# Performance work log

Measured on AMD Instinct MI355X. Metric: run time of the kernel, lower is better.

The kernel has to match this reference:

```python
import jax, jax.numpy as jnp
import numpy as np

BANDLIMIT = 0.5
STEP_SCALE = 1.0  # refiner default step_scale_value
LN_EPS = 1e-5


def _layernorm(x, g, b):
    mu = jnp.mean(x, axis=-1, keepdims=True)
    xc = x - mu
    inv = jax.lax.rsqrt(jnp.mean(xc * xc, axis=-1, keepdims=True) + LN_EPS)
    return xc * inv * g + b


def setup_inputs() -> dict:
    key = jax.random.key(0)
    ks = jax.random.split(key, 12)
    B, C, H, W = 16, 384, 64, 64
    P = 192  # conj-sym half of state_dim=384
    x = jax.random.normal(ks[0], (B, C, H, W), dtype=jnp.float32)
    ln1_g = 1.0 + 0.1 * jax.random.normal(ks[1], (C,), dtype=jnp.float32)
    ln1_b = 0.1 * jax.random.normal(ks[2], (C,), dtype=jnp.float32)
    # stable diagonal A: negative real part, HiPPO-like imaginary ladder
    lam_re = -(0.3 + jax.random.uniform(ks[3], (P,), dtype=jnp.float32))
    lam_im = jnp.pi * jnp.arange(P, dtype=jnp.float32)
    Lambda = jnp.stack([lam_re, lam_im], axis=-1)          # [P,2] (re,im)
    Bmat = jax.random.normal(ks[4], (P, C, 2), dtype=jnp.float32) / np.sqrt(C)
    Cmat = jax.random.normal(ks[5], (C, P, 2), dtype=jnp.float32) / np.sqrt(P)
    D = jax.random.normal(ks[6], (C,), dtype=jnp.float32)
    log_step = jax.random.uniform(ks[7], (P,), dtype=jnp.float32,
                                  minval=float(np.log(1e-3)), maxval=float(np.log(0.1)))
    ln2_g = 1.0 + 0.1 * jax.random.normal(ks[8], (C,), dtype=jnp.float32)
    ln2_b = 0.1 * jax.random.normal(ks[9], (C,), dtype=jnp.float32)
    W_enc = jax.random.normal(ks[10], (2 * C, C), dtype=jnp.float32) / np.sqrt(C)
    W_dec = jax.random.normal(ks[11], (C, C), dtype=jnp.float32) / np.sqrt(C)
    return {"x": x, "ln1_g": ln1_g, "ln1_b": ln1_b, "Lambda": Lambda,
            "Bmat": Bmat, "Cmat": Cmat, "D": D, "log_step": log_step,
            "ln2_g": ln2_g, "ln2_b": ln2_b, "W_enc": W_enc, "W_dec": W_dec}


def reference(x, ln1_g, ln1_b, Lambda, Bmat, Cmat, D, log_step, ln2_g, ln2_b, W_enc, W_dec):
    Bsz, C, H, W = x.shape
    u = x.reshape(Bsz, C, H * W).transpose(0, 2, 1)        # [B, L, C]

    # --- S5Block: attn branch ---
    fx = _layernorm(u, ln1_g, ln1_b)
    res = fx

    lam = Lambda[..., 0] + 1j * Lambda[..., 1]             # [P] complex
    Bc = Bmat[..., 0] + 1j * Bmat[..., 1]                  # [P, C]
    Cc = Cmat[..., 0] + 1j * Cmat[..., 1]                  # [C, P]
    step = STEP_SCALE * jnp.exp(log_step)                  # [P]
    # bandlimit mask on C (as in S5 with bandlimit=0.5)
    freqs = (step / STEP_SCALE) * jnp.abs(Lambda[..., 1]) / (2.0 * jnp.pi)
    mask = (freqs < BANDLIMIT * 0.5).astype(Cc.dtype)
    Cc = Cc * mask
    # ZOH discretization
    lam_bar = jnp.exp(lam * step)                          # [P]
    B_bar = ((lam_bar - 1.0) / lam)[:, None] * Bc          # [P, C]
    Bu = jnp.einsum('ph,blh->blp', B_bar, fx.astype(B_bar.dtype))  # [B,L,P] complex
    lam_el = jnp.broadcast_to(lam_bar, Bu.shape)

    def binop(a, b):
        # linear recurrence composition: x <- a2*(a1*x + b1) + b2
        return a[0] * b[0], b[0] * a[1] + b[1]

    _, xs = jax.lax.associative_scan(binop, (lam_el, Bu), axis=1)  # [B,L,P]
    y = 2.0 * jnp.real(jnp.einsum('hp,blp->blh', Cc, xs)) + D * fx
    y = jax.nn.gelu(y, approximate=False) + res

    # --- S5Block: GEGLU FFN branch ---
    fy = _layernorm(y, ln2_g, ln2_b)
    z = fy @ W_enc.T                                       # [B,L,2C]
    z1, z2 = jnp.split(z, 2, axis=-1)
    z = z1 * jax.nn.gelu(z2, approximate=False)
    y = z @ W_dec.T + fy

    return y.transpose(0, 2, 1).reshape(Bsz, C, H, W)
```

## Files before the change

kernel.cpp:

```cpp
#include <hip/hip_runtime.h>
#include <hip/hip_bf16.h>
#include <math.h>

typedef __attribute__((ext_vector_type(4))) float f32x4;
typedef __attribute__((ext_vector_type(8))) short s16x8;
typedef unsigned short u16;
typedef unsigned int u32;

#define CDIM 384
#define PDIM 192
#define LDIM 4096
#define BSZ  16
#define MDIM 65536
#define KD   384
#define BM 128
#define BN 128
#define BK 32
#define NT (KD / BK)
#define BUFE (BM * BK)

__device__ __forceinline__ u16 f2bf(float f) {
    u32 x = __float_as_uint(f);
    x += 0x7fffu + ((x >> 16) & 1u);
    return (u16)(x >> 16);
}
__device__ __forceinline__ float bf2f(u16 v) {
    return __uint_as_float(((u32)v) << 16);
}
__device__ __forceinline__ float gelu_exact(float x) {
    return 0.5f * x * (1.0f + erff(x * 0.7071067811865476f));
}
__device__ __forceinline__ float gelu_fast(float x) {
    float w = -1.5957691216f * x * (1.0f + 0.044715f * x * x);
    return x / (1.0f + __expf(w));
}
__device__ __forceinline__ void gld_lds16(const u16* g, u16* l) {
    __builtin_amdgcn_global_load_lds(
        (const __attribute__((address_space(1))) void*)g,
        (__attribute__((address_space(3))) void*)l, 16, 0, 0);
}

__device__ __forceinline__ void swz_decode(int NY, int& mt, int& nt) {
    int bid = blockIdx.x + gridDim.x * blockIdx.y;
    int nwg = gridDim.x * gridDim.y;
    int cpx = nwg >> 3;
    int work = (bid & 7) * cpx + (bid >> 3);
    mt = work / NY;
    nt = work - mt * NY;
}

__global__ __launch_bounds__(256) void k_setup(
    const float* __restrict__ Lambda, const float* __restrict__ Bmat,
    const float* __restrict__ Cmat, const float* __restrict__ log_step,
    const float* __restrict__ W_enc, const float* __restrict__ W_dec,
    u16* __restrict__ Wb, u16* __restrict__ Wc, u16* __restrict__ We,
    u16* __restrict__ Wd, float* __restrict__ lam_bar)
{
    int idx = blockIdx.x * 256 + threadIdx.x;
    if (idx < 73728) {
        int p = idx / CDIM, c = idx % CDIM;
        float st  = expf(log_step[p]);
        float lre = Lambda[2*p], lim = Lambda[2*p+1];
        float el  = expf(lre * st);
        float lbr = el * cosf(lim * st);
        float lbi = el * sinf(lim * st);
        float dd  = lre*lre + lim*lim;
        float a = lbr - 1.0f, b = lbi;
        float cr = (a * lre + b * lim) / dd;
        float ci = (b * lre - a * lim) / dd;
        float Br = Bmat[2*(p*CDIM + c)], Bi = Bmat[2*(p*CDIM + c) + 1];
        Wb[p*KD + c]          = f2bf(cr*Br - ci*Bi);
        Wb[(PDIM + p)*KD + c] = f2bf(cr*Bi + ci*Br);
    } else if (idx < 147456) {
        int e = idx - 73728;
        int h = e / PDIM, p = e % PDIM;
        float st  = expf(log_step[p]);
        float lim = Lambda[2*p+1];
        float freq = st * fabsf(lim) / 6.283185307179586f;
        float sc = (freq < 0.25f) ? 2.0f : 0.0f;
        Wc[h*KD + p]        = f2bf( sc * Cmat[2*(h*PDIM + p)]);
        Wc[h*KD + PDIM + p] = f2bf(-sc * Cmat[2*(h*PDIM + p) + 1]);
    } else if (idx < 442368) {
        int e = idx - 147456;
        We[e] = f2bf(W_enc[e]);
    } else if (idx < 589824) {
        int e = idx - 442368;
        Wd[e] = f2bf(W_dec[e]);
    } else if (idx < 590016) {
        int p = idx - 589824;
        float st  = expf(log_step[p]);
        float lre = Lambda[2*p], lim = Lambda[2*p+1];
        float el  = expf(lre * st);
        lam_bar[2*p]   = el * cosf(lim * st);
        lam_bar[2*p+1] = el * sinf(lim * st);
    }
}

#define LNS 388
__global__ __launch_bounds__(256) void k_ln1(
    const float* __restrict__ x, const float* __restrict__ g,
    const float* __restrict__ bb, u16* __restrict__ fx)
{
    __shared__ float tile[32 * LNS];
    __shared__ float mu_sh[32], inv_sh[32];
    int b  = blockIdx.x >> 7;
    int l0 = (blockIdx.x & 127) * 32;
    int tid = threadIdx.x;
    const float* src = x + ((size_t)b * CDIM) * LDIM + l0;
    #pragma unroll
    for (int it = 0; it < 12; it++) {
        int s = it * 256 + tid;
        int ch = s >> 3, k4 = s & 7;
        float4 v = *(const float4*)(src + (size_t)ch * LDIM + k4 * 4);
        float* t0 = tile + (k4 * 4) * LNS + ch;
        t0[0]       = v.x;
        t0[LNS]     = v.y;
        t0[2*LNS]   = v.z;
        t0[3*LNS]   = v.w;
    }
    __syncthreads();
    int j = tid >> 3, k = tid & 7;
    float sum = 0.f, sq = 0.f;
    #pragma unroll
    for (int m = 0; m < 12; m++) {
        float4 v = *(const float4*)(tile + j * LNS + (k + 8*m) * 4);
        sum += v.x + v.y + v.z + v.w;
        sq  += v.x*v.x + v.y*v.y + v.z*v.z + v.w*v.w;
    }
    sum += __shfl_xor(sum, 1); sq += __shfl_xor(sq, 1);
    sum += __shfl_xor(sum, 2); sq += __shfl_xor(sq, 2);
    sum += __shfl_xor(sum, 4); sq += __shfl_xor(sq, 4);
    float mu  = sum * (1.0f / CDIM);
    float var = sq * (1.0f / CDIM) - mu * mu;
    float inv = rsqrtf(var + 1e-5f);
    if (k == 0) { mu_sh[j] = mu; inv_sh[j] = inv; }
    __syncthreads();
    u16* dst = fx + ((size_t)(b * LDIM + l0)) * CDIM;
    #pragma unroll
    for (int it = 0; it < 12; it++) {
        int s  = it * 256 + tid;
        int cq = s % 96, jj = s / 96;
        int c  = cq * 4;
        float m2 = mu_sh[jj], iv = inv_sh[jj];
        float4 gv = *(const float4*)(g + c);
        float4 bv = *(const float4*)(bb + c);
        float4 v  = *(const float4*)(tile + jj * LNS + c);
        ushort4 o;
        o.x = f2bf((v.x - m2) * iv * gv.x + bv.x);
        o.y = f2bf((v.y - m2) * iv * gv.y + bv.y);
        o.z = f2bf((v.z - m2) * iv * gv.z + bv.z);
        o.w = f2bf((v.w - m2) * iv * gv.w + bv.w);
        *(ushort4*)(dst + (size_t)jj * CDIM + c) = o;
    }
}

template<bool SWAP>
__device__ __forceinline__ void gemm_core(
    const u16* __restrict__ A, int lda, const u16* __restrict__ Bw,
    int m0, int n0, u16* a_sh, u16* b_sh, f32x4 acc[4][4])
{
    const int tid  = threadIdx.x;
    const int w    = tid >> 6, lane = tid & 63;
    const int t16  = lane & 15, quad = lane >> 4;
    const int wm   = w >> 1,   wn   = w & 1;
    const int lr  = lane >> 2;
    const int cbg = (lane & 3) ^ ((lane >> 3) & 3);
    const u16* gA0 = A  + (size_t)(m0 + w*32 + lr) * lda + cbg*8;
    const u16* gA1 = gA0 + (size_t)16 * lda;
    const u16* gB0 = Bw + (size_t)(n0 + w*32 + lr) * KD + cbg*8;
    const u16* gB1 = gB0 + (size_t)16 * KD;
    u16* lA0 = a_sh + (w*32) * BK;
    u16* lA1 = lA0 + 16*BK;
    u16* lB0 = b_sh + (w*32) * BK;
    u16* lB1 = lB0 + 16*BK;
    const int pos = (quad ^ ((t16 >> 1) & 3)) * 8;
    const u16* ard = a_sh + (wm*64 + t16) * BK + pos;
    const u16* brd = b_sh + (wn*64 + t16) * BK + pos;
    #pragma unroll
    for (int i = 0; i < 4; i++)
        #pragma unroll
        for (int j = 0; j < 4; j++) acc[i][j] = (f32x4){0.f,0.f,0.f,0.f};
    gld_lds16(gA0, lA0);
    gld_lds16(gA1, lA1);
    gld_lds16(gB0, lB0);
    gld_lds16(gB1, lB1);
    gld_lds16(gA0 + BK, lA0 + BUFE);
    gld_lds16(gA1 + BK, lA1 + BUFE);
    gld_lds16(gB0 + BK, lB0 + BUFE);
    gld_lds16(gB1 + BK, lB1 + BUFE);
    #pragma unroll
    for (int t = 0; t < NT; ++t) {
        if (t < NT - 1) asm volatile("s_waitcnt vmcnt(4)" ::: "memory");
        else            asm volatile("s_waitcnt vmcnt(0)" ::: "memory");
        __builtin_amdgcn_s_barrier();
        __builtin_amdgcn_sched_barrier(0);
        if (t + 2 < NT) {
            const int kb = (t + 2) * BK;
            const int bo = ((t + 2) % 3) * BUFE;
            gld_lds16(gA0 + kb, lA0 + bo);
            gld_lds16(gA1 + kb, lA1 + bo);
            gld_lds16(gB0 + kb, lB0 + bo);
            gld_lds16(gB1 + kb, lB1 + bo);
        }
        __builtin_amdgcn_sched_barrier(0);
        const u16* ac = ard + (t % 3) * BUFE;
        const u16* bc = brd + (t % 3) * BUFE;
        s16x8 af[4], bfr[4];
        #pragma unroll
        for (int i = 0; i < 4; i++) af[i]  = *(const s16x8*)(ac + i*16*BK);
        #pragma unroll
        for (int j = 0; j < 4; j++) bfr[j] = *(const s16x8*)(bc + j*16*BK);
        __builtin_amdgcn_s_setprio(1);
        #pragma unroll
        for (int i = 0; i < 4; i++)
            #pragma unroll
            for (int j = 0; j < 4; j++) {
                if (SWAP)
                    acc[i][j] = __builtin_amdgcn_mfma_f32_16x16x32_bf16(bfr[j], af[i], acc[i][j], 0,0,0);
                else
                    acc[i][j] = __builtin_amdgcn_mfma_f32_16x16x32_bf16(af[i], bfr[j], acc[i][j], 0,0,0);
            }
        __builtin_amdgcn_s_setprio(0);
        asm volatile("s_waitcnt lgkmcnt(0)" ::: "memory");
        __builtin_amdgcn_sched_barrier(0);
    }
}

__global__ __launch_bounds__(256) void k_gemm_bu(
    const u16* __restrict__ fx, const u16* __restrict__ Wb, u16* __restrict__ Bu)
{
    __shared__ __align__(16) u16 a_sh[3*BUFE], b_sh[3*BUFE];
    int mt, nt;
    swz_decode(gridDim.y, mt, nt);
    int m0 = mt * BM, n0 = nt * BN;
    f32x4 acc[4][4];
    gemm_core<false>(fx, CDIM, Wb, m0, n0, a_sh, b_sh, acc);
    int lane = threadIdx.x & 63, w = threadIdx.x >> 6;
    int t16 = lane & 15, quad = lane >> 4, wm = w >> 1, wn = w & 1;
    #pragma unroll
    for (int i = 0; i < 4; i++)
        #pragma unroll
        for (int j = 0; j < 4; j++)
            #pragma unroll
            for (int rr = 0; rr < 4; rr++) {
                int m = m0 + wm*64 + i*16 + quad*4 + rr;
                int n = n0 + wn*64 + j*16 + t16;
                Bu[(size_t)m * CDIM + n] = f2bf(acc[i][j][rr]);
            }
}

__global__ __launch_bounds__(256) void k_gemm_y(
    const u16* __restrict__ xs, const u16* __restrict__ Wc,
    const u16* __restrict__ fx, const float* __restrict__ Dv, u16* __restrict__ y)
{
    __shared__ __align__(16) u16 a_sh[3*BUFE], b_sh[3*BUFE];
    int mt, nt;
    swz_decode(gridDim.y, mt, nt);
    int m0 = mt * BM, n0 = nt * BN;
    f32x4 acc[4][4];
    gemm_core<false>(xs, CDIM, Wc, m0, n0, a_sh, b_sh, acc);
    int lane = threadIdx.x & 63, w = threadIdx.x >> 6;
    int t16 = lane & 15, quad = lane >> 4, wm = w >> 1, wn = w & 1;
    float dv[4];
    #pragma unroll
    for (int j = 0; j < 4; j++) dv[j] = Dv[n0 + wn*64 + j*16 + t16];
    #pragma unroll
    for (int i = 0; i < 4; i++)
        #pragma unroll
        for (int j = 0; j < 4; j++)
            #pragma unroll
            for (int rr = 0; rr < 4; rr++) {
                int m = m0 + wm*64 + i*16 + quad*4 + rr;
                int n = n0 + wn*64 + j*16 + t16;
                float fxv = bf2f(fx[(size_t)m * CDIM + n]);
                float v = acc[i][j][rr] + dv[j] * fxv;
                y[(size_t)m * CDIM + n] = f2bf(gelu_fast(v) + fxv);
            }
}

__global__ __launch_bounds__(256) void k_gemm_zg(
    const u16* __restrict__ fy, const u16* __restrict__ We, u16* __restrict__ zg)
{
    __shared__ __align__(16) u16 sh[6*BUFE];
    u16* a_sh = sh;
    u16* b_sh = sh + 3*BUFE;
    const int tid = threadIdx.x;
    const int w = tid >> 6, lane = tid & 63;
    const int t16 = lane & 15, quad = lane >> 4;
    const int wm = w >> 1, wn = w & 1;
    int mt, nt;
    swz_decode(gridDim.y, mt, nt);
    const int m0 = mt * BM;
    const int c0 = nt * 64;
    const int lr  = lane >> 2;
    const int cbg = (lane & 3) ^ ((lane >> 3) & 3);
    const u16* gA0 = fy + (size_t)(m0 + w*32 + lr) * CDIM + cbg*8;
    const u16* gA1 = gA0 + (size_t)16 * CDIM;
    int brow = c0 + w*32 + ((w >= 2) ? 320 : 0);
    const u16* gB0 = We + (size_t)(brow + lr) * KD + cbg*8;
    const u16* gB1 = gB0 + (size_t)16 * KD;
    u16* lA0 = a_sh + (w*32) * BK;
    u16* lA1 = lA0 + 16*BK;
    u16* lB0 = b_sh + (w*32) * BK;
    u16* lB1 = lB0 + 16*BK;
    const int pos = (quad ^ ((t16 >> 1) & 3)) * 8;
    const u16* ard = a_sh + (wm*64 + t16) * BK + pos;
    const u16* brd = b_sh + (wn*64 + t16) * BK + pos;
    f32x4 acc[4][4];
    #pragma unroll
    for (int i = 0; i < 4; i++)
        #pragma unroll
        for (int j = 0; j < 4; j++) acc[i][j] = (f32x4){0.f,0.f,0.f,0.f};
    gld_lds16(gA0, lA0);
    gld_lds16(gA1, lA1);
    gld_lds16(gB0, lB0);
    gld_lds16(gB1, lB1);
    gld_lds16(gA0 + BK, lA0 + BUFE);
    gld_lds16(gA1 + BK, lA1 + BUFE);
    gld_lds16(gB0 + BK, lB0 + BUFE);
    gld_lds16(gB1 + BK, lB1 + BUFE);
    #pragma unroll
    for (int t = 0; t < NT; ++t) {
        if (t < NT - 1) asm volatile("s_waitcnt vmcnt(4)" ::: "memory");
        else            asm volatile("s_waitcnt vmcnt(0)" ::: "memory");
        __builtin_amdgcn_s_barrier();
        __builtin_amdgcn_sched_barrier(0);
        if (t + 2 < NT) {
            const int kb = (t + 2) * BK;
            const int bo = ((t + 2) % 3) * BUFE;
            gld_lds16(gA0 + kb, lA0 + bo);
            gld_lds16(gA1 + kb, lA1 + bo);
            gld_lds16(gB0 + kb, lB0 + bo);
            gld_lds16(gB1 + kb, lB1 + bo);
        }
        __builtin_amdgcn_sched_barrier(0);
        const u16* ac = ard + (t % 3) * BUFE;
        const u16* bc = brd + (t % 3) * BUFE;
        s16x8 af[4], bfr[4];
        #pragma unroll
        for (int i = 0; i < 4; i++) af[i]  = *(const s16x8*)(ac + i*16*BK);
        #pragma unroll
        for (int j = 0; j < 4; j++) bfr[j] = *(const s16x8*)(bc + j*16*BK);
        __builtin_amdgcn_s_setprio(1);
        #pragma unroll
        for (int i = 0; i < 4; i++)
            #pragma unroll
            for (int j = 0; j < 4; j++)
                acc[i][j] = __builtin_amdgcn_mfma_f32_16x16x32_bf16(af[i], bfr[j], acc[i][j], 0,0,0);
        __builtin_amdgcn_s_setprio(0);
        asm volatile("s_waitcnt lgkmcnt(0)" ::: "memory");
        __builtin_amdgcn_sched_barrier(0);
    }
    __syncthreads();
    if (wn == 1) {
        #pragma unroll
        for (int i = 0; i < 4; i++)
            #pragma unroll
            for (int j = 0; j < 4; j++)
                #pragma unroll
                for (int rr = 0; rr < 4; rr++) {
                    int m = wm*64 + i*16 + quad*4 + rr;
                    int c = j*16 + t16;
                    sh[m*66 + c] = f2bf(gelu_fast(acc[i][j][rr]));
                }
    }
    __syncthreads();
    if (wn == 0) {
        #pragma unroll
        for (int i = 0; i < 4; i++)
            #pragma unroll
            for (int j = 0; j < 4; j++)
                #pragma unroll
                for (int rr = 0; rr < 4; rr++) {
                    int m = wm*64 + i*16 + quad*4 + rr;
                    int c = j*16 + t16;
                    float gv = bf2f(sh[m*66 + c]);
                    zg[(size_t)(m0 + m) * CDIM + c0 + c] = f2bf(acc[i][j][rr] * gv);
                }
    }
}

__global__ __launch_bounds__(256) void k_gemm_out(
    const u16* __restrict__ zg, const u16* __restrict__ Wd,
    const u16* __restrict__ fy, float* __restrict__ out)
{
    __shared__ __align__(16) u16 a_sh[3*BUFE], b_sh[3*BUFE];
    int mt, nt;
    swz_decode(gridDim.y, mt, nt);
    int m0 = mt * BM, n0 = nt * BN;
    f32x4 acc[4][4];
    gemm_core<true>(zg, CDIM, Wd, m0, n0, a_sh, b_sh, acc);
    int lane = threadIdx.x & 63, w = threadIdx.x >> 6;
    int t16 = lane & 15, quad = lane >> 4, wm = w >> 1, wn = w & 1;
    int b = m0 >> 12;
    #pragma unroll
    for (int i = 0; i < 4; i++)
        #pragma unroll
        for (int j = 0; j < 4; j++)
            #pragma unroll
            for (int rr = 0; rr < 4; rr++) {
                int nn = n0 + wn*64 + j*16 + quad*4 + rr;
                int mm = m0 + wm*64 + i*16 + t16;
                float fyv = bf2f(fy[(size_t)mm * CDIM + nn]);
                int l = mm & 4095;
                out[((size_t)(b * CDIM + nn)) * LDIM + l] = acc[i][j][rr] + fyv;
            }
}

__global__ __launch_bounds__(192) void k_scan_a(
    const u16* __restrict__ Bu, const float* __restrict__ lam_bar,
    float* __restrict__ summ)
{
    int b = blockIdx.x >> 6, ch = blockIdx.x & 63;
    int p = threadIdx.x;
    float lr = lam_bar[2*p], li = lam_bar[2*p+1];
    float xr = 0.f, xi = 0.f;
    const u16* base = Bu + (size_t)(b * LDIM + ch * 64) * CDIM;
    #pragma unroll 8
    for (int i = 0; i < 64; i++) {
        float br = bf2f(base[(size_t)i * CDIM + p]);
        float bi = bf2f(base[(size_t)i * CDIM + PDIM + p]);
        float nr = lr * xr - li * xi + br;
        float ni = lr * xi + li * xr + bi;
        xr = nr; xi = ni;
    }
    size_t o = (size_t)(b * 64 + ch) * CDIM + p;
    summ[o] = xr;
    summ[o + PDIM] = xi;
}

__global__ __launch_bounds__(256) void k_scan_b(
    const float* __restrict__ lam_bar, float* __restrict__ summ)
{
    int id = blockIdx.x * 256 + threadIdx.x;
    if (id >= BSZ * PDIM) return;
    int b = id / PDIM, p = id % PDIM;
    float ar = lam_bar[2*p], ai = lam_bar[2*p+1];
    #pragma unroll
    for (int s = 0; s < 6; s++) {
        float nr = ar * ar - ai * ai, ni = 2.f * ar * ai;
        ar = nr; ai = ni;
    }
    float cr = 0.f, ci = 0.f;
    #pragma unroll 4
    for (int ch = 0; ch < 64; ch++) {
        size_t o = (size_t)(b * 64 + ch) * CDIM + p;
        float sr = summ[o], si = summ[o + PDIM];
        summ[o] = cr; summ[o + PDIM] = ci;
        float nr = ar * cr - ai * ci + sr;
        float ni = ar * ci + ai * cr + si;
        cr = nr; ci = ni;
    }
}

__global__ __launch_bounds__(192) void k_scan_c(
    u16* __restrict__ Bu, const float* __restrict__ lam_bar,
    const float* __restrict__ summ)
{
    int b = blockIdx.x >> 6, ch = blockIdx.x & 63;
    int p = threadIdx.x;
    float lr = lam_bar[2*p], li = lam_bar[2*p+1];
    size_t oc = (size_t)(b * 64 + ch) * CDIM + p;
    float xr = summ[oc], xi = summ[oc + PDIM];
    u16* base = Bu + (size_t)(b * LDIM + ch * 64) * CDIM;
    #pragma unroll 8
    for (int i = 0; i < 64; i++) {
        float br = bf2f(base[(size_t)i * CDIM + p]);
        float bi = bf2f(base[(size_t)i * CDIM + PDIM + p]);
        float nr = lr * xr - li * xi + br;
        float ni = lr * xi + li * xr + bi;
        xr = nr; xi = ni;
        base[(size_t)i * CDIM + p] = f2bf(xr);
        base[(size_t)i * CDIM + PDIM + p] = f2bf(xi);
    }
}

__global__ __launch_bounds__(256) void k_ln2(
    const u16* __restrict__ y, const float* __restrict__ g,
    const float* __restrict__ bb, u16* __restrict__ fy)
{
    int w = threadIdx.x >> 6, lane = threadIdx.x & 63;
    size_t m = (size_t)blockIdx.x * 4 + w;
    const u16* row = y + m * CDIM;
    float v[6];
    float sum = 0.f, sq = 0.f;
    #pragma unroll
    for (int i = 0; i < 6; i++) {
        v[i] = bf2f(row[lane + 64 * i]);
        sum += v[i]; sq += v[i] * v[i];
    }
    #pragma unroll
    for (int o = 1; o < 64; o <<= 1) {
        sum += __shfl_xor(sum, o); sq += __shfl_xor(sq, o);
    }
    float mu  = sum * (1.0f / CDIM);
    float var = sq * (1.0f / CDIM) - mu * mu;
    float inv = rsqrtf(var + 1e-5f);
    u16* dst = fy + m * CDIM;
    #pragma unroll
    for (int i = 0; i < 6; i++) {
        int c = lane + 64 * i;
        dst[c] = f2bf((v[i] - mu) * inv * g[c] + bb[c]);
    }
}

extern "C" void kernel_launch(void* const* d_in, const int* in_sizes, int n_in,
                              void* d_out, int out_size, void* d_ws, size_t ws_size,
                              hipStream_t stream)
{
    const float* x        = (const float*)d_in[0];
    const float* ln1_g    = (const float*)d_in[1];
    const float* ln1_b    = (const float*)d_in[2];
    const float* Lambda   = (const float*)d_in[3];
    const float* Bmat     = (const float*)d_in[4];
    const float* Cmat     = (const float*)d_in[5];
    const float* Dvec     = (const float*)d_in[6];
    const float* log_step = (const float*)d_in[7];
    const float* ln2_g    = (const float*)d_in[8];
    const float* ln2_b    = (const float*)d_in[9];
    const float* W_enc    = (const float*)d_in[10];
    const float* W_dec    = (const float*)d_in[11];

    char* ws = (char*)d_ws;
    const size_t HBF = (size_t)MDIM * CDIM * 2;
    u16* fx = (u16*)(ws);
    u16* fy = (u16*)(ws + HBF);
    u16* bu = (u16*)(ws + 2 * HBF);
    u16* zg = (u16*)(ws + 2 * HBF);
    char* wbase = ws + 3 * HBF;
    u16* Wb = (u16*)(wbase);
    u16* Wc = (u16*)(wbase + 294912);
    u16* We = (u16*)(wbase + 589824);
    u16* Wd = (u16*)(wbase + 1179648);
    float* lam_bar = (float*)(wbase + 1474560);
    float* summ    = (float*)(wbase + 1476096);
    u16* yb  = (u16*)d_out;
    float* out = (float*)d_out;

    k_setup<<<2305, 256, 0, stream>>>(Lambda, Bmat, Cmat, log_step, W_enc, W_dec,
                                      Wb, Wc, We, Wd, lam_bar);
    k_ln1<<<2048, 256, 0, stream>>>(x, ln1_g, ln1_b, fx);
    k_gemm_bu<<<dim3(512, 3), 256, 0, stream>>>(fx, Wb, bu);
    k_scan_a<<<1024, 192, 0, stream>>>(bu, lam_bar, summ);
    k_scan_b<<<12, 256, 0, stream>>>(lam_bar, summ);
    k_scan_c<<<1024, 192, 0, stream>>>(bu, lam_bar, summ);
    k_gemm_y<<<dim3(512, 3), 256, 0, stream>>>(bu, Wc, fx, Dvec, yb);
    k_ln2<<<16384, 256, 0, stream>>>(yb, ln2_g, ln2_b, fy);
    k_gemm_zg<<<dim3(512, 6), 256, 0, stream>>>(fy, We, zg);
    k_gemm_out<<<dim3(512, 3), 256, 0, stream>>>(zg, Wd, fy, out);
}
```

Measured before the change: 423.0 us.

## Load GEMM weight fragments directly into registers instead of staging through LDS

All four GEMM kernels now fetch their B-operand (weight) fragments straight from global memory into registers, double-buffered one K-step ahead, and no longer copy them into LDS. Only the activation tile is staged in shared memory. This halves LDS footprint and LDS read traffic, which can raise occupancy. The cost is four uncoalesced 16-byte global loads per lane per step, relying on the small weights being cache-resident, and the vmcnt wait counts are retuned to match.

```diff
diff --git a/kernel.cpp b/kernel.cpp
--- a/kernel.cpp
+++ b/kernel.cpp
@@ -157,7 +157,7 @@
 template<bool SWAP>
 __device__ __forceinline__ void gemm_core(
     const u16* __restrict__ A, int lda, const u16* __restrict__ Bw,
-    int m0, int n0, u16* a_sh, u16* b_sh, f32x4 acc[4][4])
+    int m0, int n0, u16* a_sh, f32x4 acc[4][4])
 {
     const int tid  = threadIdx.x;
     const int w    = tid >> 6, lane = tid & 63;
@@ -167,31 +167,26 @@
     const int cbg = (lane & 3) ^ ((lane >> 3) & 3);
     const u16* gA0 = A  + (size_t)(m0 + w*32 + lr) * lda + cbg*8;
     const u16* gA1 = gA0 + (size_t)16 * lda;
-    const u16* gB0 = Bw + (size_t)(n0 + w*32 + lr) * KD + cbg*8;
-    const u16* gB1 = gB0 + (size_t)16 * KD;
     u16* lA0 = a_sh + (w*32) * BK;
     u16* lA1 = lA0 + 16*BK;
-    u16* lB0 = b_sh + (w*32) * BK;
-    u16* lB1 = lB0 + 16*BK;
     const int pos = (quad ^ ((t16 >> 1) & 3)) * 8;
     const u16* ard = a_sh + (wm*64 + t16) * BK + pos;
-    const u16* brd = b_sh + (wn*64 + t16) * BK + pos;
+    const u16* gB = Bw + (size_t)(n0 + wn*64 + t16) * KD + quad*8;
     #pragma unroll
     for (int i = 0; i < 4; i++)
         #pragma unroll
         for (int j = 0; j < 4; j++) acc[i][j] = (f32x4){0.f,0.f,0.f,0.f};
     gld_lds16(gA0, lA0);
     gld_lds16(gA1, lA1);
-    gld_lds16(gB0, lB0);
-    gld_lds16(gB1, lB1);
     gld_lds16(gA0 + BK, lA0 + BUFE);
     gld_lds16(gA1 + BK, lA1 + BUFE);
-    gld_lds16(gB0 + BK, lB0 + BUFE);
-    gld_lds16(gB1 + BK, lB1 + BUFE);
+    s16x8 bq[2][4];
+    #pragma unroll
+    for (int j = 0; j < 4; j++) bq[0][j] = *(const s16x8*)(gB + (size_t)j * 16 * KD);
     #pragma unroll
     for (int t = 0; t < NT; ++t) {
-        if (t < NT - 1) asm volatile("s_waitcnt vmcnt(4)" ::: "memory");
-        else            asm volatile("s_waitcnt vmcnt(0)" ::: "memory");
+        if (t < NT - 1) asm volatile("s_waitcnt vmcnt(6)" ::: "memory");
+        else            asm volatile("s_waitcnt vmcnt(4)" ::: "memory");
         __builtin_amdgcn_s_barrier();
         __builtin_amdgcn_sched_barrier(0);
         if (t + 2 < NT) {
@@ -199,26 +194,26 @@
             const int bo = ((t + 2) % 3) * BUFE;
             gld_lds16(gA0 + kb, lA0 + bo);
             gld_lds16(gA1 + kb, lA1 + bo);
-            gld_lds16(gB0 + kb, lB0 + bo);
-            gld_lds16(gB1 + kb, lB1 + bo);
+        }
+        if (t + 1 < NT) {
+            #pragma unroll
+            for (int j = 0; j < 4; j++)
+                bq[(t + 1) & 1][j] = *(const s16x8*)(gB + (size_t)j * 16 * KD + (t + 1) * BK);
         }
         __builtin_amdgcn_sched_barrier(0);
         const u16* ac = ard + (t % 3) * BUFE;
-        const u16* bc = brd + (t % 3) * BUFE;
-        s16x8 af[4], bfr[4];
-        #pragma unroll
-        for (int i = 0; i < 4; i++) af[i]  = *(const s16x8*)(ac + i*16*BK);
-        #pragma unroll
-        for (int j = 0; j < 4; j++) bfr[j] = *(const s16x8*)(bc + j*16*BK);
+        s16x8 af[4];
+        #pragma unroll
+        for (int i = 0; i < 4; i++) af[i] = *(const s16x8*)(ac + i*16*BK);
         __builtin_amdgcn_s_setprio(1);
         #pragma unroll
         for (int i = 0; i < 4; i++)
             #pragma unroll
             for (int j = 0; j < 4; j++) {
                 if (SWAP)
-                    acc[i][j] = __builtin_amdgcn_mfma_f32_16x16x32_bf16(bfr[j], af[i], acc[i][j], 0,0,0);
+                    acc[i][j] = __builtin_amdgcn_mfma_f32_16x16x32_bf16(bq[t & 1][j], af[i], acc[i][j], 0,0,0);
                 else
-                    acc[i][j] = __builtin_amdgcn_mfma_f32_16x16x32_bf16(af[i], bfr[j], acc[i][j], 0,0,0);
+                    acc[i][j] = __builtin_amdgcn_mfma_f32_16x16x32_bf16(af[i], bq[t & 1][j], acc[i][j], 0,0,0);
             }
         __builtin_amdgcn_s_setprio(0);
         asm volatile("s_waitcnt lgkmcnt(0)" ::: "memory");
@@ -229,12 +224,12 @@
 __global__ __launch_bounds__(256) void k_gemm_bu(
     const u16* __restrict__ fx, const u16* __restrict__ Wb, u16* __restrict__ Bu)
 {
-    __shared__ __align__(16) u16 a_sh[3*BUFE], b_sh[3*BUFE];
+    __shared__ __align__(16) u16 a_sh[3*BUFE];
     int mt, nt;
     swz_decode(gridDim.y, mt, nt);
     int m0 = mt * BM, n0 = nt * BN;
     f32x4 acc[4][4];
-    gemm_core<false>(fx, CDIM, Wb, m0, n0, a_sh, b_sh, acc);
+    gemm_core<false>(fx, CDIM, Wb, m0, n0, a_sh, acc);
     int lane = threadIdx.x & 63, w = threadIdx.x >> 6;
     int t16 = lane & 15, quad = lane >> 4, wm = w >> 1, wn = w & 1;
     #pragma unroll
@@ -253,12 +248,12 @@
     const u16* __restrict__ xs, const u16* __restrict__ Wc,
     const u16* __restrict__ fx, const float* __restrict__ Dv, u16* __restrict__ y)
 {
-    __shared__ __align__(16) u16 a_sh[3*BUFE], b_sh[3*BUFE];
+    __shared__ __align__(16) u16 a_sh[3*BUFE];
     int mt, nt;
     swz_decode(gridDim.y, mt, nt);
     int m0 = mt * BM, n0 = nt * BN;
     f32x4 acc[4][4];
-    gemm_core<false>(xs, CDIM, Wc, m0, n0, a_sh, b_sh, acc);
+    gemm_core<false>(xs, CDIM, Wc, m0, n0, a_sh, acc);
     int lane = threadIdx.x & 63, w = threadIdx.x >> 6;
     int t16 = lane & 15, quad = lane >> 4, wm = w >> 1, wn = w & 1;
     float dv[4];
@@ -281,9 +276,7 @@
 __global__ __launch_bounds__(256) void k_gemm_zg(
     const u16* __restrict__ fy, const u16* __restrict__ We, u16* __restrict__ zg)
 {
-    __shared__ __align__(16) u16 sh[6*BUFE];
-    u16* a_sh = sh;
-    u16* b_sh = sh + 3*BUFE;
+    __shared__ __align__(16) u16 sh[3*BUFE];
     const int tid = threadIdx.x;
     const int w = tid >> 6, lane = tid & 63;
     const int t16 = lane & 15, quad = lane >> 4;
@@ -296,16 +289,11 @@
     const int cbg = (lane & 3) ^ ((lane >> 3) & 3);
     const u16* gA0 = fy + (size_t)(m0 + w*32 + lr) * CDIM + cbg*8;
     const u16* gA1 = gA0 + (size_t)16 * CDIM;
-    int brow = c0 + w*32 + ((w >= 2) ? 320 : 0);
-    const u16* gB0 = We + (size_t)(brow + lr) * KD + cbg*8;
-    const u16* gB1 = gB0 + (size_t)16 * KD;
-    u16* lA0 = a_sh + (w*32) * BK;
+    u16* lA0 = sh + (w*32) * BK;
     u16* lA1 = lA0 + 16*BK;
-    u16* lB0 = b_sh + (w*32) * BK;
-    u16* lB1 = lB0 + 16*BK;
     const int pos = (quad ^ ((t16 >> 1) & 3)) * 8;
-    const u16* ard = a_sh + (wm*64 + t16) * BK + pos;
-    const u16* brd = b_sh + (wn*64 + t16) * BK + pos;
+    const u16* ard = sh + (wm*64 + t16) * BK + pos;
+    const u16* gB = We + (size_t)(c0 + wn*384 + t16) * KD + quad*8;
     f32x4 acc[4][4];
     #pragma unroll
     for (int i = 0; i < 4; i++)
@@ -313,16 +301,15 @@
         for (int j = 0; j < 4; j++) acc[i][j] = (f32x4){0.f,0.f,0.f,0.f};
     gld_lds16(gA0, lA0);
     gld_lds16(gA1, lA1);
-    gld_lds16(gB0, lB0);
-    gld_lds16(gB1, lB1);
     gld_lds16(gA0 + BK, lA0 + BUFE);
     gld_lds16(gA1 + BK, lA1 + BUFE);
-    gld_lds16(gB0 + BK, lB0 + BUFE);
-    gld_lds16(gB1 + BK, lB1 + BUFE);
+    s16x8 bq[2][4];
+    #pragma unroll
+    for (int j = 0; j < 4; j++) bq[0][j] = *(const s16x8*)(gB + (size_t)j * 16 * KD);
     #pragma unroll
     for (int t = 0; t < NT; ++t) {
-        if (t < NT - 1) asm volatile("s_waitcnt vmcnt(4)" ::: "memory");
-        else            asm volatile("s_waitcnt vmcnt(0)" ::: "memory");
+        if (t < NT - 1) asm volatile("s_waitcnt vmcnt(6)" ::: "memory");
+        else            asm volatile("s_waitcnt vmcnt(4)" ::: "memory");
         __builtin_amdgcn_s_barrier();
         __builtin_amdgcn_sched_barrier(0);
         if (t + 2 < NT) {
@@ -330,23 +317,23 @@
             const int bo = ((t + 2) % 3) * BUFE;
             gld_lds16(gA0 + kb, lA0 + bo);
             gld_lds16(gA1 + kb, lA1 + bo);
-            gld_lds16(gB0 + kb, lB0 + bo);
-            gld_lds16(gB1 + kb, lB1 + bo);
+        }
+        if (t + 1 < NT) {
+            #pragma unroll
+            for (int j = 0; j < 4; j++)
+                bq[(t + 1) & 1][j] = *(const s16x8*)(gB + (size_t)j * 16 * KD + (t + 1) * BK);
         }
         __builtin_amdgcn_sched_barrier(0);
         const u16* ac = ard + (t % 3) * BUFE;
-        const u16* bc = brd + (t % 3) * BUFE;
-        s16x8 af[4], bfr[4];
-        #pragma unroll
-        for (int i = 0; i < 4; i++) af[i]  = *(const s16x8*)(ac + i*16*BK);
-        #pragma unroll
-        for (int j = 0; j < 4; j++) bfr[j] = *(const s16x8*)(bc + j*16*BK);
+        s16x8 af[4];
+        #pragma unroll
+        for (int i = 0; i < 4; i++) af[i] = *(const s16x8*)(ac + i*16*BK);
         __builtin_amdgcn_s_setprio(1);
         #pragma unroll
         for (int i = 0; i < 4; i++)
             #pragma unroll
             for (int j = 0; j < 4; j++)
-                acc[i][j] = __builtin_amdgcn_mfma_f32_16x16x32_bf16(af[i], bfr[j], acc[i][j], 0,0,0);
+                acc[i][j] = __builtin_amdgcn_mfma_f32_16x16x32_bf16(af[i], bq[t & 1][j], acc[i][j], 0,0,0);
         __builtin_amdgcn_s_setprio(0);
         asm volatile("s_waitcnt lgkmcnt(0)" ::: "memory");
         __builtin_amdgcn_sched_barrier(0);
@@ -384,12 +371,12 @@
     const u16* __restrict__ zg, const u16* __restrict__ Wd,
     const u16* __restrict__ fy, float* __restrict__ out)
 {
-    __shared__ __align__(16) u16 a_sh[3*BUFE], b_sh[3*BUFE];
+    __shared__ __align__(16) u16 a_sh[3*BUFE];
     int mt, nt;
     swz_decode(gridDim.y, mt, nt);
     int m0 = mt * BM, n0 = nt * BN;
     f32x4 acc[4][4];
-    gemm_core<true>(zg, CDIM, Wd, m0, n0, a_sh, b_sh, acc);
+    gemm_core<true>(zg, CDIM, Wd, m0, n0, a_sh, acc);
     int lane = threadIdx.x & 63, w = threadIdx.x >> 6;
     int t16 = lane & 15, quad = lane >> 4, wm = w >> 1, wn = w & 1;
     int b = m0 >> 12;
```

Result: slower. 489.3 us (+15.7%).

## Double-buffer B tiles, stream A fragments, and vectorize LN2 loads

Applied to the files above, without the earlier changes.

The GEMM mainloop now keeps A in a triple buffer but B in a double buffer, prefetching B one step ahead and A two steps ahead. This cuts LDS per block from six buffers to five. A fragments are loaded one row-block at a time inside the MFMA loop to lower register pressure, and launch_bounds now request 4 blocks per SM. LN2 reads and writes bf16 pairs as 32-bit words with float2 gamma/beta loads. The trade-off is less prefetch slack for B, plus a possible stall on the per-iteration A loads.

```diff
diff --git a/kernel.cpp b/kernel.cpp
--- a/kernel.cpp
+++ b/kernel.cpp
@@ -186,50 +186,50 @@
     gld_lds16(gB1, lB1);
     gld_lds16(gA0 + BK, lA0 + BUFE);
     gld_lds16(gA1 + BK, lA1 + BUFE);
-    gld_lds16(gB0 + BK, lB0 + BUFE);
-    gld_lds16(gB1 + BK, lB1 + BUFE);
     #pragma unroll
     for (int t = 0; t < NT; ++t) {
-        if (t < NT - 1) asm volatile("s_waitcnt vmcnt(4)" ::: "memory");
+        if (t < NT - 1) asm volatile("s_waitcnt vmcnt(2)" ::: "memory");
         else            asm volatile("s_waitcnt vmcnt(0)" ::: "memory");
         __builtin_amdgcn_s_barrier();
         __builtin_amdgcn_sched_barrier(0);
-        if (t + 2 < NT) {
-            const int kb = (t + 2) * BK;
-            const int bo = ((t + 2) % 3) * BUFE;
-            gld_lds16(gA0 + kb, lA0 + bo);
-            gld_lds16(gA1 + kb, lA1 + bo);
+        if (t + 1 < NT) {
+            const int kb = (t + 1) * BK, bo = ((t + 1) & 1) * BUFE;
             gld_lds16(gB0 + kb, lB0 + bo);
             gld_lds16(gB1 + kb, lB1 + bo);
         }
+        if (t + 2 < NT) {
+            const int kb = (t + 2) * BK, ao = ((t + 2) % 3) * BUFE;
+            gld_lds16(gA0 + kb, lA0 + ao);
+            gld_lds16(gA1 + kb, lA1 + ao);
+        }
         __builtin_amdgcn_sched_barrier(0);
         const u16* ac = ard + (t % 3) * BUFE;
-        const u16* bc = brd + (t % 3) * BUFE;
-        s16x8 af[4], bfr[4];
-        #pragma unroll
-        for (int i = 0; i < 4; i++) af[i]  = *(const s16x8*)(ac + i*16*BK);
+        const u16* bc = brd + (t & 1) * BUFE;
+        s16x8 bfr[4];
         #pragma unroll
         for (int j = 0; j < 4; j++) bfr[j] = *(const s16x8*)(bc + j*16*BK);
         __builtin_amdgcn_s_setprio(1);
         #pragma unroll
-        for (int i = 0; i < 4; i++)
+        for (int i = 0; i < 4; i++) {
+            s16x8 af = *(const s16x8*)(ac + i*16*BK);
             #pragma unroll
             for (int j = 0; j < 4; j++) {
                 if (SWAP)
-                    acc[i][j] = __builtin_amdgcn_mfma_f32_16x16x32_bf16(bfr[j], af[i], acc[i][j], 0,0,0);
+                    acc[i][j] = __builtin_amdgcn_mfma_f32_16x16x32_bf16(bfr[j], af, acc[i][j], 0,0,0);
                 else
-                    acc[i][j] = __builtin_amdgcn_mfma_f32_16x16x32_bf16(af[i], bfr[j], acc[i][j], 0,0,0);
+                    acc[i][j] = __builtin_amdgcn_mfma_f32_16x16x32_bf16(af, bfr[j], acc[i][j], 0,0,0);
             }
+        }
         __builtin_amdgcn_s_setprio(0);
         asm volatile("s_waitcnt lgkmcnt(0)" ::: "memory");
         __builtin_amdgcn_sched_barrier(0);
     }
 }
 
-__global__ __launch_bounds__(256) void k_gemm_bu(
+__global__ __launch_bounds__(256, 4) void k_gemm_bu(
     const u16* __restrict__ fx, const u16* __restrict__ Wb, u16* __restrict__ Bu)
 {
-    __shared__ __align__(16) u16 a_sh[3*BUFE], b_sh[3*BUFE];
+    __shared__ __align__(16) u16 a_sh[3*BUFE], b_sh[2*BUFE];
     int mt, nt;
     swz_decode(gridDim.y, mt, nt);
     int m0 = mt * BM, n0 = nt * BN;
@@ -249,11 +249,11 @@
             }
 }
 
-__global__ __launch_bounds__(256) void k_gemm_y(
+__global__ __launch_bounds__(256, 4) void k_gemm_y(
     const u16* __restrict__ xs, const u16* __restrict__ Wc,
     const u16* __restrict__ fx, const float* __restrict__ Dv, u16* __restrict__ y)
 {
-    __shared__ __align__(16) u16 a_sh[3*BUFE], b_sh[3*BUFE];
+    __shared__ __align__(16) u16 a_sh[3*BUFE], b_sh[2*BUFE];
     int mt, nt;
     swz_decode(gridDim.y, mt, nt);
     int m0 = mt * BM, n0 = nt * BN;
@@ -278,10 +278,10 @@
             }
 }
 
-__global__ __launch_bounds__(256) void k_gemm_zg(
+__global__ __launch_bounds__(256, 4) void k_gemm_zg(
     const u16* __restrict__ fy, const u16* __restrict__ We, u16* __restrict__ zg)
 {
-    __shared__ __align__(16) u16 sh[6*BUFE];
+    __shared__ __align__(16) u16 sh[5*BUFE];
     u16* a_sh = sh;
     u16* b_sh = sh + 3*BUFE;
     const int tid = threadIdx.x;
@@ -317,36 +317,36 @@
     gld_lds16(gB1, lB1);
     gld_lds16(gA0 + BK, lA0 + BUFE);
     gld_lds16(gA1 + BK, lA1 + BUFE);
-    gld_lds16(gB0 + BK, lB0 + BUFE);
-    gld_lds16(gB1 + BK, lB1 + BUFE);
     #pragma unroll
     for (int t = 0; t < NT; ++t) {
-        if (t < NT - 1) asm volatile("s_waitcnt vmcnt(4)" ::: "memory");
+        if (t < NT - 1) asm volatile("s_waitcnt vmcnt(2)" ::: "memory");
         else            asm volatile("s_waitcnt vmcnt(0)" ::: "memory");
         __builtin_amdgcn_s_barrier();
         __builtin_amdgcn_sched_barrier(0);
-        if (t + 2 < NT) {
-            const int kb = (t + 2) * BK;
-            const int bo = ((t + 2) % 3) * BUFE;
-            gld_lds16(gA0 + kb, lA0 + bo);
-            gld_lds16(gA1 + kb, lA1 + bo);
+        if (t + 1 < NT) {
+            const int kb = (t + 1) * BK, bo = ((t + 1) & 1) * BUFE;
             gld_lds16(gB0 + kb, lB0 + bo);
             gld_lds16(gB1 + kb, lB1 + bo);
         }
+        if (t + 2 < NT) {
+            const int kb = (t + 2) * BK, ao = ((t + 2) % 3) * BUFE;
+            gld_lds16(gA0 + kb, lA0 + ao);
+            gld_lds16(gA1 + kb, lA1 + ao);
+        }
         __builtin_amdgcn_sched_barrier(0);
         const u16* ac = ard + (t % 3) * BUFE;
-        const u16* bc = brd + (t % 3) * BUFE;
-        s16x8 af[4], bfr[4];
-        #pragma unroll
-        for (int i = 0; i < 4; i++) af[i]  = *(const s16x8*)(ac + i*16*BK);
+        const u16* bc = brd + (t & 1) * BUFE;
+        s16x8 bfr[4];
         #pragma unroll
         for (int j = 0; j < 4; j++) bfr[j] = *(const s16x8*)(bc + j*16*BK);
         __builtin_amdgcn_s_setprio(1);
         #pragma unroll
-        for (int i = 0; i < 4; i++)
+        for (int i = 0; i < 4; i++) {
+            s16x8 af = *(const s16x8*)(ac + i*16*BK);
             #pragma unroll
             for (int j = 0; j < 4; j++)
-                acc[i][j] = __builtin_amdgcn_mfma_f32_16x16x32_bf16(af[i], bfr[j], acc[i][j], 0,0,0);
+                acc[i][j] = __builtin_amdgcn_mfma_f32_16x16x32_bf16(af, bfr[j], acc[i][j], 0,0,0);
+        }
         __builtin_amdgcn_s_setprio(0);
         asm volatile("s_waitcnt lgkmcnt(0)" ::: "memory");
         __builtin_amdgcn_sched_barrier(0);
@@ -380,11 +380,11 @@
     }
 }
 
-__global__ __launch_bounds__(256) void k_gemm_out(
+__global__ __launch_bounds__(256, 4) void k_gemm_out(
     const u16* __restrict__ zg, const u16* __restrict__ Wd,
     const u16* __restrict__ fy, float* __restrict__ out)
 {
-    __shared__ __align__(16) u16 a_sh[3*BUFE], b_sh[3*BUFE];
+    __shared__ __align__(16) u16 a_sh[3*BUFE], b_sh[2*BUFE];
     int mt, nt;
     swz_decode(gridDim.y, mt, nt);
     int m0 = mt * BM, n0 = nt * BN;
@@ -485,9 +485,11 @@
     float v[6];
     float sum = 0.f, sq = 0.f;
     #pragma unroll
-    for (int i = 0; i < 6; i++) {
-        v[i] = bf2f(row[lane + 64 * i]);
-        sum += v[i]; sq += v[i] * v[i];
+    for (int i = 0; i < 3; i++) {
+        u32 pk = *(const u32*)(row + lane * 2 + 128 * i);
+        float a = bf2f((u16)pk), b2 = bf2f((u16)(pk >> 16));
+        v[2*i] = a; v[2*i+1] = b2;
+        sum += a + b2; sq += a*a + b2*b2;
     }
     #pragma unroll
     for (int o = 1; o < 64; o <<= 1) {
@@ -498,9 +500,13 @@
     float inv = rsqrtf(var + 1e-5f);
     u16* dst = fy + m * CDIM;
     #pragma unroll
-    for (int i = 0; i < 6; i++) {
-        int c = lane + 64 * i;
-        dst[c] = f2bf((v[i] - mu) * inv * g[c] + bb[c]);
+    for (int i = 0; i < 3; i++) {
+        int c = lane * 2 + 128 * i;
+        float2 gv = *(const float2*)(g + c);
+        float2 bv = *(const float2*)(bb + c);
+        u16 o0 = f2bf((v[2*i]   - mu) * inv * gv.x + bv.x);
+        u16 o1 = f2bf((v[2*i+1] - mu) * inv * gv.y + bv.y);
+        *(u32*)(dst + c) = (u32)o0 | ((u32)o1 << 16);
     }
 }
 
```

Measured after the change: 421.9 us. Within noise of the previous version (-0.3%).
